# Kernel tuning notes

Measured on AMD Instinct MI355X. Metric: run time of the kernel, lower is better.

Reference implementation:

```python
import jax, jax.numpy as jnp
import numpy as np

B, S, D = 2, 2048, 1024
H, DH = 16, 64
DM = 4096  # d_mlp = 4*d_model
EPS = 1e-5


def setup_inputs() -> dict:
    key = jax.random.key(0)
    ks = jax.random.split(key, 16)
    s = 0.02
    return {
        "resid_pre": jax.random.normal(ks[0], (B, S, D), jnp.float32),
        "ln1_w": jnp.ones((D,), jnp.float32),
        "ln1_b": jnp.zeros((D,), jnp.float32),
        "W_Q": jax.random.normal(ks[1], (H, D, DH), jnp.float32) * s,
        "W_K": jax.random.normal(ks[2], (H, D, DH), jnp.float32) * s,
        "W_V": jax.random.normal(ks[3], (H, D, DH), jnp.float32) * s,
        "W_O": jax.random.normal(ks[4], (H, DH, D), jnp.float32) * s,
        "b_Q": jnp.zeros((H, DH), jnp.float32),
        "b_K": jnp.zeros((H, DH), jnp.float32),
        "b_V": jnp.zeros((H, DH), jnp.float32),
        "b_O": jnp.zeros((D,), jnp.float32),
        "ln2_w": jnp.ones((D,), jnp.float32),
        "ln2_b": jnp.zeros((D,), jnp.float32),
        "W_in": jax.random.normal(ks[5], (D, DM), jnp.float32) * s,
        "b_in": jnp.zeros((DM,), jnp.float32),
        "W_out": jax.random.normal(ks[6], (DM, D), jnp.float32) * s,
        "b_out": jnp.zeros((D,), jnp.float32),
    }


def _layernorm(x, w, b):
    # TransformerLens LayerNorm: center, scale by sqrt(mean(x^2)+eps), affine
    x = x - x.mean(-1, keepdims=True)
    scale = jnp.sqrt((x * x).mean(-1, keepdims=True) + EPS)
    return x / scale * w + b


def _attention(x, W_Q, W_K, W_V, W_O, b_Q, b_K, b_V, b_O):
    # q,k,v: [batch, pos, head, d_head]
    q = jnp.einsum('bpd,hdk->bphk', x, W_Q) + b_Q
    k = jnp.einsum('bpd,hdk->bphk', x, W_K) + b_K
    v = jnp.einsum('bpd,hdk->bphk', x, W_V) + b_V
    attn_scale = jnp.float32(np.sqrt(DH))
    # scores: [batch, head, query_pos, key_pos]
    scores = jnp.einsum('bqhk,bphk->bhqp', q, k) / attn_scale
    causal = jnp.tril(jnp.ones((S, S), bool))
    scores = jnp.where(causal[None, None, :, :], scores, -jnp.inf)
    pattern = jax.nn.softmax(scores, axis=-1)
    pattern = jnp.where(jnp.isnan(pattern), 0.0, pattern)
    z = jnp.einsum('bphk,bhqp->bqhk', v, pattern)
    return jnp.einsum('bqhk,hkd->bqd', z, W_O) + b_O


def _mlp(x, W_in, b_in, W_out, b_out):
    pre = jnp.einsum('bpd,dm->bpm', x, W_in) + b_in
    post = jax.nn.gelu(pre, approximate=True)  # gelu_new (tanh approx)
    return jnp.einsum('bpm,md->bpd', post, W_out) + b_out


def reference(resid_pre, ln1_w, ln1_b, W_Q, W_K, W_V, W_O, b_Q, b_K, b_V, b_O,
              ln2_w, ln2_b, W_in, b_in, W_out, b_out):
    attn_out = _attention(_layernorm(resid_pre, ln1_w, ln1_b),
                          W_Q, W_K, W_V, W_O, b_Q, b_K, b_V, b_O)
    resid_mid = resid_pre + attn_out
    mlp_out = _mlp(_layernorm(resid_mid, ln2_w, ln2_b), W_in, b_in, W_out, b_out)
    return resid_mid + mlp_out
```

## Files before the change

### kernel.cpp

```cpp
#include <hip/hip_runtime.h>
#include <cstdint>
#include <cstddef>

#define SEQ    2048
#define DMODEL 1024
#define NHEAD  16
#define DHEAD  64
#define DMLP   4096
#define ROWS   4096

typedef __attribute__((ext_vector_type(8))) short bf16x8v;
typedef __attribute__((ext_vector_type(4))) float f32x4;

__device__ __forceinline__ float wave_reduce_sum(float v) {
#pragma unroll
  for (int off = 32; off; off >>= 1) v += __shfl_xor(v, off, 64);
  return v;
}
__device__ __forceinline__ float gelu_new(float x) {
  const float c = 0.7978845608028654f;
  float inner = c * (x + 0.044715f * x * x * x);
  return 0.5f * x * (1.0f + tanhf(inner));
}
__device__ __forceinline__ unsigned short f2bf(float x) {
  union { float f; unsigned u; } v; v.f = x;
  unsigned r = v.u + 0x7fffu + ((v.u >> 16) & 1u);
  return (unsigned short)(r >> 16);
}
__device__ __forceinline__ void gload_lds16(const void* g, void* l) {
  __builtin_amdgcn_global_load_lds(
      (const __attribute__((address_space(1))) unsigned int*)g,
      (__attribute__((address_space(3))) unsigned int*)l, 16, 0, 0);
}

__global__ __launch_bounds__(256)
void ln_bf16_kernel(const float* __restrict__ x, const float* __restrict__ w,
                    const float* __restrict__ b, unsigned short* __restrict__ y) {
  __shared__ float sred[4];
  const int r = blockIdx.x;
  const int t = threadIdx.x;
  const int wid = t >> 6, lane = t & 63;
  const float4 v = ((const float4*)(x + (size_t)r * DMODEL))[t];

  float s = v.x + v.y + v.z + v.w;
  s = wave_reduce_sum(s);
  if (lane == 0) sred[wid] = s;
  __syncthreads();
  const float mean = (sred[0] + sred[1] + sred[2] + sred[3]) * (1.0f / DMODEL);
  __syncthreads();

  float4 c;
  c.x = v.x - mean; c.y = v.y - mean; c.z = v.z - mean; c.w = v.w - mean;
  float ss = c.x * c.x + c.y * c.y + c.z * c.z + c.w * c.w;
  ss = wave_reduce_sum(ss);
  if (lane == 0) sred[wid] = ss;
  __syncthreads();
  const float rs =
      rsqrtf((sred[0] + sred[1] + sred[2] + sred[3]) * (1.0f / DMODEL) + 1e-5f);

  const float4 wv = ((const float4*)w)[t];
  const float4 bv = ((const float4*)b)[t];
  ushort4 o;
  o.x = f2bf(c.x * rs * wv.x + bv.x);
  o.y = f2bf(c.y * rs * wv.y + bv.y);
  o.z = f2bf(c.z * rs * wv.z + bv.z);
  o.w = f2bf(c.w * rs * wv.w + bv.w);
  ((ushort4*)(y + (size_t)r * DMODEL))[t] = o;
}

__global__ __launch_bounds__(256)
void transpose_cvt(const float* __restrict__ src, unsigned short* __restrict__ dst,
                   int ld_src, int ld_dst) {
  __shared__ float t[64][68];
  const int r0 = blockIdx.y * 64, c0 = blockIdx.x * 64;
  const int tid = threadIdx.x;
  const int c4 = (tid & 15) * 4, r = tid >> 4;
#pragma unroll
  for (int p = 0; p < 4; ++p) {
    const float4 v = *(const float4*)(src + (size_t)(r0 + r + p * 16) * ld_src + c0 + c4);
    *(float4*)&t[r + p * 16][c4] = v;
  }
  __syncthreads();
  const int r4 = (tid & 15) * 4, c = tid >> 4;
#pragma unroll
  for (int p = 0; p < 4; ++p) {
    const int cc = c + p * 16;
    ushort4 o;
    o.x = f2bf(t[r4 + 0][cc]);
    o.y = f2bf(t[r4 + 1][cc]);
    o.z = f2bf(t[r4 + 2][cc]);
    o.w = f2bf(t[r4 + 3][cc]);
    *(ushort4*)(dst + (size_t)(c0 + cc) * ld_dst + r0 + r4) = o;
  }
}

__global__ __launch_bounds__(256)
void cvt_wqkv(const float* __restrict__ Wq, const float* __restrict__ Wk,
              const float* __restrict__ Wv, unsigned short* __restrict__ out) {
  __shared__ float t[64][68];
  const float* src = (blockIdx.z == 0) ? Wq : (blockIdx.z == 1) ? Wk : Wv;
  unsigned short* dst = out + (size_t)blockIdx.z * (DMODEL * NHEAD * DHEAD);
  const int h = blockIdx.y, d0 = blockIdx.x * 64;
  const int tid = threadIdx.x;
  const int c4 = (tid & 15) * 4, r = tid >> 4;
#pragma unroll
  for (int p = 0; p < 4; ++p) {
    const float4 v = *(const float4*)(src + (size_t)h * (DMODEL * DHEAD) +
                                      (size_t)(d0 + r + p * 16) * DHEAD + c4);
    *(float4*)&t[r + p * 16][c4] = v;
  }
  __syncthreads();
  const int r4 = (tid & 15) * 4, c = tid >> 4;
#pragma unroll
  for (int p = 0; p < 4; ++p) {
    const int cc = c + p * 16;
    ushort4 o;
    o.x = f2bf(t[r4 + 0][cc]);
    o.y = f2bf(t[r4 + 1][cc]);
    o.z = f2bf(t[r4 + 2][cc]);
    o.w = f2bf(t[r4 + 3][cc]);
    *(ushort4*)(dst + (size_t)(h * 64 + cc) * DMODEL + d0 + r4) = o;
  }
}

template <int EPI>
__global__ __launch_bounds__(256)
void gemm_bf16(const unsigned short* __restrict__ A,
               const unsigned short* __restrict__ Bt,
               const float* __restrict__ bias, const float* __restrict__ addend,
               void* __restrict__ Cout, int ldc, int K) {
  __shared__ unsigned short As[128 * 32];
  __shared__ unsigned short Bs[128 * 32];
  const int tid = threadIdx.x;
  const int w = tid >> 6, lane = tid & 63;
  const int wr = w >> 1, wc = w & 1;
  const int m0 = blockIdx.x * 128, n0 = blockIdx.y * 128;

  f32x4 acc[4][4];
#pragma unroll
  for (int m = 0; m < 4; ++m)
#pragma unroll
    for (int n = 0; n < 4; ++n) acc[m][n] = (f32x4){0.f, 0.f, 0.f, 0.f};

  const int srow = w * 32 + (lane >> 2);
  const int scol = (lane & 3) * 8;

  for (int k0 = 0; k0 < K; k0 += 32) {
    __syncthreads();
#pragma unroll
    for (int it = 0; it < 2; ++it) {
      const int row = srow + it * 16;
      gload_lds16(A + (size_t)(m0 + row) * K + k0 + scol,
                  &As[(w * 32 + it * 16) * 32]);
      gload_lds16(Bt + (size_t)(n0 + row) * K + k0 + scol,
                  &Bs[(w * 32 + it * 16) * 32]);
    }
    __syncthreads();

    bf16x8v af[4], bf[4];
#pragma unroll
    for (int m = 0; m < 4; ++m)
      af[m] = *(const bf16x8v*)&As[(wr * 64 + m * 16 + (lane & 15)) * 32 + (lane >> 4) * 8];
#pragma unroll
    for (int n = 0; n < 4; ++n)
      bf[n] = *(const bf16x8v*)&Bs[(wc * 64 + n * 16 + (lane & 15)) * 32 + (lane >> 4) * 8];
#pragma unroll
    for (int m = 0; m < 4; ++m)
#pragma unroll
      for (int n = 0; n < 4; ++n)
        acc[m][n] = __builtin_amdgcn_mfma_f32_16x16x32_bf16(af[m], bf[n], acc[m][n], 0, 0, 0);
  }

#pragma unroll
  for (int m = 0; m < 4; ++m) {
    const int row = m0 + wr * 64 + m * 16 + (lane >> 4) * 4;
#pragma unroll
    for (int n = 0; n < 4; ++n) {
      const int col = n0 + wc * 64 + n * 16 + (lane & 15);
      const float bcol = bias[col];
      const f32x4 a = acc[m][n];
      if (EPI == 4) {
        ushort4 o;
        o.x = f2bf(a[0] + bcol); o.y = f2bf(a[1] + bcol);
        o.z = f2bf(a[2] + bcol); o.w = f2bf(a[3] + bcol);
        *(ushort4*)((unsigned short*)Cout + (size_t)col * ldc + row) = o;
      } else {
#pragma unroll
        for (int r = 0; r < 4; ++r) {
          const float val = a[r] + bcol;
          const size_t off = (size_t)(row + r) * ldc + col;
          if (EPI == 0) {
            ((float*)Cout)[off] = val;
          } else if (EPI == 1) {
            ((unsigned short*)Cout)[off] = f2bf(gelu_new(val));
          } else if (EPI == 2) {
            ((float*)Cout)[off] = val + addend[off];
          } else if (EPI == 3) {
            ((float*)Cout)[off] += val;
          } else {
            ((unsigned short*)Cout)[off] = f2bf(val);
          }
        }
      }
    }
  }
}

__global__ __launch_bounds__(256)
void attn_mfma_kernel(const unsigned short* __restrict__ Qb,
                      const unsigned short* __restrict__ Kb,
                      const unsigned short* __restrict__ Vt,
                      unsigned short* __restrict__ Zb) {
  __shared__ unsigned short Ps[4][16][72];
  const int tid = threadIdx.x;
  const int w = tid >> 6, lane = tid & 63;
  const int lg = lane >> 4, lr = lane & 15;
  const int bh = blockIdx.x >> 4;
  const int pr = blockIdx.x & 15;
  const int h = bh & 15, b = bh >> 4;
  const size_t qk_base = (size_t)b * SEQ * DMODEL + (size_t)h * DHEAD;
  const size_t vt_base = (size_t)(h * DHEAD) * ROWS + (size_t)b * SEQ;

#pragma unroll
  for (int sel = 0; sel < 2; ++sel) {
    const int qblk = sel ? (31 - pr) : pr;
    const int q0 = qblk * 64 + w * 16;
    const int myq = q0 + lr;

    bf16x8v bq[2];
#pragma unroll
    for (int ks = 0; ks < 2; ++ks)
      bq[ks] = *(const bf16x8v*)&Qb[qk_base + (size_t)myq * DMODEL + ks * 32 + lg * 8];

    f32x4 accz[4];
#pragma unroll
    for (int nd = 0; nd < 4; ++nd) accz[nd] = (f32x4){0.f, 0.f, 0.f, 0.f};
    float mq = -3.0e38f, Lq = 0.0f;

    for (int jc = 0; jc <= qblk * 64; jc += 64) {
      f32x4 accs[4];
#pragma unroll
      for (int n = 0; n < 4; ++n) accs[n] = (f32x4){0.f, 0.f, 0.f, 0.f};
#pragma unroll
      for (int ks = 0; ks < 2; ++ks) {
#pragma unroll
        for (int n = 0; n < 4; ++n) {
          const bf16x8v bk = *(const bf16x8v*)
              &Kb[qk_base + (size_t)(jc + n * 16 + lr) * DMODEL + ks * 32 + lg * 8];
          accs[n] = __builtin_amdgcn_mfma_f32_16x16x32_bf16(bk, bq[ks], accs[n], 0, 0, 0);
        }
      }
      float mx = -3.0e38f;
#pragma unroll
      for (int n = 0; n < 4; ++n) {
#pragma unroll
        for (int r = 0; r < 4; ++r) {
          float s = accs[n][r] * 0.125f;
          s = (jc + n * 16 + 4 * lg + r <= myq) ? s : -3.0e38f;
          accs[n][r] = s;
          mx = fmaxf(mx, s);
        }
      }
      mx = fmaxf(mx, __shfl_xor(mx, 16, 64));
      mx = fmaxf(mx, __shfl_xor(mx, 32, 64));
      const float mn = fmaxf(mq, mx);
      const float c0 = __expf(mq - mn);
      float sum = 0.0f;
#pragma unroll
      for (int n = 0; n < 4; ++n) {
#pragma unroll
        for (int r = 0; r < 4; ++r) {
          const float pp = __expf(accs[n][r] - mn);
          sum += pp;
          Ps[w][lr][n * 16 + 4 * lg + r] = f2bf(pp);
        }
      }
      sum += __shfl_xor(sum, 16, 64);
      sum += __shfl_xor(sum, 32, 64);
      Lq = Lq * c0 + sum;
      mq = mn;
#pragma unroll
      for (int nd = 0; nd < 4; ++nd) accz[nd] *= c0;
      bf16x8v ap[2];
#pragma unroll
      for (int ks = 0; ks < 2; ++ks)
        ap[ks] = *(const bf16x8v*)&Ps[w][lr][ks * 32 + lg * 8];
#pragma unroll
      for (int ks = 0; ks < 2; ++ks) {
#pragma unroll
        for (int nd = 0; nd < 4; ++nd) {
          const bf16x8v bv = *(const bf16x8v*)
              &Vt[vt_base + (size_t)(nd * 16 + lr) * ROWS + jc + ks * 32 + lg * 8];
          accz[nd] = __builtin_amdgcn_mfma_f32_16x16x32_bf16(bv, ap[ks], accz[nd], 0, 0, 0);
        }
      }
    }
    const float rL = 1.0f / Lq;
    unsigned short* zrow = Zb + (size_t)((size_t)b * SEQ + myq) * DMODEL + h * DHEAD;
#pragma unroll
    for (int nd = 0; nd < 4; ++nd) {
      ushort4 o;
      o.x = f2bf(accz[nd][0] * rL);
      o.y = f2bf(accz[nd][1] * rL);
      o.z = f2bf(accz[nd][2] * rL);
      o.w = f2bf(accz[nd][3] * rL);
      *(ushort4*)(zrow + nd * 16 + 4 * lg) = o;
    }
  }
}

extern "C" void kernel_launch(void* const* d_in, const int* in_sizes, int n_in,
                              void* d_out, int out_size, void* d_ws, size_t ws_size,
                              hipStream_t stream) {
  const float* resid_pre = (const float*)d_in[0];
  const float* ln1_w = (const float*)d_in[1];
  const float* ln1_b = (const float*)d_in[2];
  const float* W_Q = (const float*)d_in[3];
  const float* W_K = (const float*)d_in[4];
  const float* W_V = (const float*)d_in[5];
  const float* W_O = (const float*)d_in[6];
  const float* b_Q = (const float*)d_in[7];
  const float* b_K = (const float*)d_in[8];
  const float* b_V = (const float*)d_in[9];
  const float* b_O = (const float*)d_in[10];
  const float* ln2_w = (const float*)d_in[11];
  const float* ln2_b = (const float*)d_in[12];
  const float* W_in = (const float*)d_in[13];
  const float* b_in = (const float*)d_in[14];
  const float* W_out = (const float*)d_in[15];
  const float* b_out = (const float*)d_in[16];
  (void)in_sizes; (void)n_in; (void)out_size; (void)ws_size;

  float* out = (float*)d_out;
  char* w8 = (char*)d_ws;
  unsigned short* xln_b = (unsigned short*)(w8);
  unsigned short* Zb    = (unsigned short*)(w8);
  unsigned short* WQt   = (unsigned short*)(w8 + (8u << 20));
  unsigned short* WOt   = (unsigned short*)(w8 + (14u << 20));
  unsigned short* Wint  = (unsigned short*)(w8 + (16u << 20));
  unsigned short* Woutt = (unsigned short*)(w8 + (24u << 20));
  unsigned short* Qb    = (unsigned short*)(w8 + (32u << 20));
  unsigned short* Kb    = (unsigned short*)(w8 + (40u << 20));
  unsigned short* Vt    = (unsigned short*)(w8 + (48u << 20));
  unsigned short* hid_b = (unsigned short*)(w8 + (32u << 20));

  cvt_wqkv<<<dim3(16, 16, 3), 256, 0, stream>>>(W_Q, W_K, W_V, WQt);
  transpose_cvt<<<dim3(16, 16), 256, 0, stream>>>(W_O, WOt, DMODEL, DMODEL);
  transpose_cvt<<<dim3(64, 16), 256, 0, stream>>>(W_in, Wint, DMLP, DMODEL);
  transpose_cvt<<<dim3(16, 64), 256, 0, stream>>>(W_out, Woutt, DMODEL, DMLP);

  ln_bf16_kernel<<<ROWS, 256, 0, stream>>>(resid_pre, ln1_w, ln1_b, xln_b);
  dim3 g1024(ROWS / 128, 1024 / 128);
  gemm_bf16<5><<<g1024, 256, 0, stream>>>(xln_b, WQt, b_Q, nullptr, Qb, DMODEL, DMODEL);
  gemm_bf16<5><<<g1024, 256, 0, stream>>>(xln_b, WQt + (1u << 20), b_K, nullptr, Kb, DMODEL, DMODEL);
  gemm_bf16<4><<<g1024, 256, 0, stream>>>(xln_b, WQt + (2u << 20), b_V, nullptr, Vt, ROWS, DMODEL);
  attn_mfma_kernel<<<512, 256, 0, stream>>>(Qb, Kb, Vt, Zb);
  gemm_bf16<2><<<g1024, 256, 0, stream>>>(Zb, WOt, b_O, resid_pre, out, DMODEL, DMODEL);
  ln_bf16_kernel<<<ROWS, 256, 0, stream>>>(out, ln2_w, ln2_b, xln_b);
  dim3 gin(ROWS / 128, DMLP / 128);
  gemm_bf16<1><<<gin, 256, 0, stream>>>(xln_b, Wint, b_in, nullptr, hid_b, DMLP, DMODEL);
  gemm_bf16<3><<<g1024, 256, 0, stream>>>(hid_b, Woutt, b_out, nullptr, out, DMODEL, DMLP);
}
```

Measured before the change: 553.9 us.

## Fuse QKV projections into one GEMM and software-pipeline attention K/V loads

Replaces three separate Q, K and V GEMM launches with one gemm_qkv kernel over a 24-column-block grid that picks bias and output layout per block. In the attention kernel, it prefetches the next K tile into registers and loads V before the softmax to hide global latency, and applies the causal mask only on the diagonal tile. It also packs the P stores into ushort4 writes and reorders block indexing so neighbouring blocks share a query-block pair. The costs are higher register pressure from the prefetch buffers, and a QKV GEMM whose single-buffered LDS loop may run slower than the existing gemm_bf16.

```diff
diff --git a/kernel.cpp b/kernel.cpp
--- a/kernel.cpp
+++ b/kernel.cpp
@@ -207,6 +207,80 @@
 }
 
 __global__ __launch_bounds__(256)
+void gemm_qkv(const unsigned short* __restrict__ A,
+              const unsigned short* __restrict__ Bt,
+              const float* __restrict__ bQ, const float* __restrict__ bK,
+              const float* __restrict__ bV,
+              unsigned short* __restrict__ Qb, unsigned short* __restrict__ Kb,
+              unsigned short* __restrict__ Vt) {
+  __shared__ unsigned short As[128 * 32];
+  __shared__ unsigned short Bs[128 * 32];
+  const int tid = threadIdx.x;
+  const int w = tid >> 6, lane = tid & 63;
+  const int wr = w >> 1, wc = w & 1;
+  const int m0 = blockIdx.x * 128, n0 = blockIdx.y * 128;
+
+  f32x4 acc[4][4];
+#pragma unroll
+  for (int m = 0; m < 4; ++m)
+#pragma unroll
+    for (int n = 0; n < 4; ++n) acc[m][n] = (f32x4){0.f, 0.f, 0.f, 0.f};
+
+  const int srow = w * 32 + (lane >> 2);
+  const int scol = (lane & 3) * 8;
+
+  for (int k0 = 0; k0 < DMODEL; k0 += 32) {
+    __syncthreads();
+#pragma unroll
+    for (int it = 0; it < 2; ++it) {
+      const int row = srow + it * 16;
+      gload_lds16(A + (size_t)(m0 + row) * DMODEL + k0 + scol,
+                  &As[(w * 32 + it * 16) * 32]);
+      gload_lds16(Bt + (size_t)(n0 + row) * DMODEL + k0 + scol,
+                  &Bs[(w * 32 + it * 16) * 32]);
+    }
+    __syncthreads();
+
+    bf16x8v af[4], bf[4];
+#pragma unroll
+    for (int m = 0; m < 4; ++m)
+      af[m] = *(const bf16x8v*)&As[(wr * 64 + m * 16 + (lane & 15)) * 32 + (lane >> 4) * 8];
+#pragma unroll
+    for (int n = 0; n < 4; ++n)
+      bf[n] = *(const bf16x8v*)&Bs[(wc * 64 + n * 16 + (lane & 15)) * 32 + (lane >> 4) * 8];
+#pragma unroll
+    for (int m = 0; m < 4; ++m)
+#pragma unroll
+      for (int n = 0; n < 4; ++n)
+        acc[m][n] = __builtin_amdgcn_mfma_f32_16x16x32_bf16(af[m], bf[n], acc[m][n], 0, 0, 0);
+  }
+
+  const int which = blockIdx.y >> 3;
+  const float* bias = (which == 0) ? bQ : (which == 1) ? bK : bV;
+#pragma unroll
+  for (int m = 0; m < 4; ++m) {
+    const int row = m0 + wr * 64 + m * 16 + (lane >> 4) * 4;
+#pragma unroll
+    for (int n = 0; n < 4; ++n) {
+      const int col = (n0 + wc * 64 + n * 16 + (lane & 15)) & 1023;
+      const float bcol = bias[col];
+      const f32x4 a = acc[m][n];
+      if (which == 2) {
+        ushort4 o;
+        o.x = f2bf(a[0] + bcol); o.y = f2bf(a[1] + bcol);
+        o.z = f2bf(a[2] + bcol); o.w = f2bf(a[3] + bcol);
+        *(ushort4*)(Vt + (size_t)col * ROWS + row) = o;
+      } else {
+        unsigned short* dst = which ? Kb : Qb;
+#pragma unroll
+        for (int r = 0; r < 4; ++r)
+          dst[(size_t)(row + r) * DMODEL + col] = f2bf(a[r] + bcol);
+      }
+    }
+  }
+}
+
+__global__ __launch_bounds__(256)
 void attn_mfma_kernel(const unsigned short* __restrict__ Qb,
                       const unsigned short* __restrict__ Kb,
                       const unsigned short* __restrict__ Vt,
@@ -215,17 +289,17 @@
   const int tid = threadIdx.x;
   const int w = tid >> 6, lane = tid & 63;
   const int lg = lane >> 4, lr = lane & 15;
-  const int bh = blockIdx.x >> 4;
-  const int pr = blockIdx.x & 15;
+  const int bh = blockIdx.x & 31;
+  const int pr = blockIdx.x >> 5;
   const int h = bh & 15, b = bh >> 4;
   const size_t qk_base = (size_t)b * SEQ * DMODEL + (size_t)h * DHEAD;
   const size_t vt_base = (size_t)(h * DHEAD) * ROWS + (size_t)b * SEQ;
 
-#pragma unroll
   for (int sel = 0; sel < 2; ++sel) {
     const int qblk = sel ? (31 - pr) : pr;
     const int q0 = qblk * 64 + w * 16;
     const int myq = q0 + lr;
+    const int jlast = qblk * 64;
 
     bf16x8v bq[2];
 #pragma unroll
@@ -237,29 +311,59 @@
     for (int nd = 0; nd < 4; ++nd) accz[nd] = (f32x4){0.f, 0.f, 0.f, 0.f};
     float mq = -3.0e38f, Lq = 0.0f;
 
-    for (int jc = 0; jc <= qblk * 64; jc += 64) {
+    bf16x8v kf[2][4];
+#pragma unroll
+    for (int ks = 0; ks < 2; ++ks)
+#pragma unroll
+      for (int n = 0; n < 4; ++n)
+        kf[ks][n] = *(const bf16x8v*)
+            &Kb[qk_base + (size_t)(n * 16 + lr) * DMODEL + ks * 32 + lg * 8];
+
+    for (int jc = 0; jc <= jlast; jc += 64) {
       f32x4 accs[4];
 #pragma unroll
       for (int n = 0; n < 4; ++n) accs[n] = (f32x4){0.f, 0.f, 0.f, 0.f};
 #pragma unroll
-      for (int ks = 0; ks < 2; ++ks) {
-#pragma unroll
-        for (int n = 0; n < 4; ++n) {
-          const bf16x8v bk = *(const bf16x8v*)
-              &Kb[qk_base + (size_t)(jc + n * 16 + lr) * DMODEL + ks * 32 + lg * 8];
-          accs[n] = __builtin_amdgcn_mfma_f32_16x16x32_bf16(bk, bq[ks], accs[n], 0, 0, 0);
-        }
+      for (int ks = 0; ks < 2; ++ks)
+#pragma unroll
+        for (int n = 0; n < 4; ++n)
+          accs[n] = __builtin_amdgcn_mfma_f32_16x16x32_bf16(kf[ks][n], bq[ks], accs[n], 0, 0, 0);
+
+      const int jn = jc + 64;
+      if (jn <= jlast) {
+#pragma unroll
+        for (int ks = 0; ks < 2; ++ks)
+#pragma unroll
+          for (int n = 0; n < 4; ++n)
+            kf[ks][n] = *(const bf16x8v*)
+                &Kb[qk_base + (size_t)(jn + n * 16 + lr) * DMODEL + ks * 32 + lg * 8];
       }
+      bf16x8v vf[2][4];
+#pragma unroll
+      for (int ks = 0; ks < 2; ++ks)
+#pragma unroll
+        for (int nd = 0; nd < 4; ++nd)
+          vf[ks][nd] = *(const bf16x8v*)
+              &Vt[vt_base + (size_t)(nd * 16 + lr) * ROWS + jc + ks * 32 + lg * 8];
+
       float mx = -3.0e38f;
-#pragma unroll
-      for (int n = 0; n < 4; ++n) {
-#pragma unroll
-        for (int r = 0; r < 4; ++r) {
-          float s = accs[n][r] * 0.125f;
-          s = (jc + n * 16 + 4 * lg + r <= myq) ? s : -3.0e38f;
-          accs[n][r] = s;
-          mx = fmaxf(mx, s);
-        }
+      if (jc == jlast) {
+#pragma unroll
+        for (int n = 0; n < 4; ++n)
+#pragma unroll
+          for (int r = 0; r < 4; ++r) {
+            float s = accs[n][r] * 0.125f;
+            s = (jc + n * 16 + 4 * lg + r <= myq) ? s : -3.0e38f;
+            accs[n][r] = s; mx = fmaxf(mx, s);
+          }
+      } else {
+#pragma unroll
+        for (int n = 0; n < 4; ++n)
+#pragma unroll
+          for (int r = 0; r < 4; ++r) {
+            const float s = accs[n][r] * 0.125f;
+            accs[n][r] = s; mx = fmaxf(mx, s);
+          }
       }
       mx = fmaxf(mx, __shfl_xor(mx, 16, 64));
       mx = fmaxf(mx, __shfl_xor(mx, 32, 64));
@@ -268,12 +372,12 @@
       float sum = 0.0f;
 #pragma unroll
       for (int n = 0; n < 4; ++n) {
-#pragma unroll
-        for (int r = 0; r < 4; ++r) {
-          const float pp = __expf(accs[n][r] - mn);
-          sum += pp;
-          Ps[w][lr][n * 16 + 4 * lg + r] = f2bf(pp);
-        }
+        ushort4 pk;
+        float e0 = __expf(accs[n][0] - mn), e1 = __expf(accs[n][1] - mn);
+        float e2 = __expf(accs[n][2] - mn), e3 = __expf(accs[n][3] - mn);
+        sum += e0 + e1 + e2 + e3;
+        pk.x = f2bf(e0); pk.y = f2bf(e1); pk.z = f2bf(e2); pk.w = f2bf(e3);
+        *(ushort4*)&Ps[w][lr][n * 16 + 4 * lg] = pk;
       }
       sum += __shfl_xor(sum, 16, 64);
       sum += __shfl_xor(sum, 32, 64);
@@ -286,14 +390,10 @@
       for (int ks = 0; ks < 2; ++ks)
         ap[ks] = *(const bf16x8v*)&Ps[w][lr][ks * 32 + lg * 8];
 #pragma unroll
-      for (int ks = 0; ks < 2; ++ks) {
-#pragma unroll
-        for (int nd = 0; nd < 4; ++nd) {
-          const bf16x8v bv = *(const bf16x8v*)
-              &Vt[vt_base + (size_t)(nd * 16 + lr) * ROWS + jc + ks * 32 + lg * 8];
-          accz[nd] = __builtin_amdgcn_mfma_f32_16x16x32_bf16(bv, ap[ks], accz[nd], 0, 0, 0);
-        }
-      }
+      for (int ks = 0; ks < 2; ++ks)
+#pragma unroll
+        for (int nd = 0; nd < 4; ++nd)
+          accz[nd] = __builtin_amdgcn_mfma_f32_16x16x32_bf16(vf[ks][nd], ap[ks], accz[nd], 0, 0, 0);
     }
     const float rL = 1.0f / Lq;
     unsigned short* zrow = Zb + (size_t)((size_t)b * SEQ + myq) * DMODEL + h * DHEAD;
@@ -350,11 +450,9 @@
   transpose_cvt<<<dim3(16, 64), 256, 0, stream>>>(W_out, Woutt, DMODEL, DMLP);
 
   ln_bf16_kernel<<<ROWS, 256, 0, stream>>>(resid_pre, ln1_w, ln1_b, xln_b);
+  gemm_qkv<<<dim3(32, 24), 256, 0, stream>>>(xln_b, WQt, b_Q, b_K, b_V, Qb, Kb, Vt);
+  attn_mfma_kernel<<<512, 256, 0, stream>>>(Qb, Kb, Vt, Zb);
   dim3 g1024(ROWS / 128, 1024 / 128);
-  gemm_bf16<5><<<g1024, 256, 0, stream>>>(xln_b, WQt, b_Q, nullptr, Qb, DMODEL, DMODEL);
-  gemm_bf16<5><<<g1024, 256, 0, stream>>>(xln_b, WQt + (1u << 20), b_K, nullptr, Kb, DMODEL, DMODEL);
-  gemm_bf16<4><<<g1024, 256, 0, stream>>>(xln_b, WQt + (2u << 20), b_V, nullptr, Vt, ROWS, DMODEL);
-  attn_mfma_kernel<<<512, 256, 0, stream>>>(Qb, Kb, Vt, Zb);
   gemm_bf16<2><<<g1024, 256, 0, stream>>>(Zb, WOt, b_O, resid_pre, out, DMODEL, DMODEL);
   ln_bf16_kernel<<<ROWS, 256, 0, stream>>>(out, ln2_w, ln2_b, xln_b);
   dim3 gin(ROWS / 128, DMLP / 128);
```

After: 502.5 us. -9.3%, faster.
